# Kernel optimization log

Hardware: AMD Instinct MI355X
Metric: run time of the kernel (lower is better)

Reference implementation:

```python
import jax, jax.numpy as jnp
import numpy as np
from jax.scipy.special import logsumexp


def _lstm(x, mask, Wk, Wr, b, reverse=False):
    # x: [B,T,D], mask: [B,T] bool. Keras LSTM defaults: gate order i,f,g,o,
    # sigmoid recurrent activation, tanh activation. Masked steps carry state.
    if reverse:
        x = x[:, ::-1]
        mask = mask[:, ::-1]
    B, T, _ = x.shape
    H = Wr.shape[0]
    xz = jnp.einsum('btd,dh->bth', x, Wk) + b  # [B,T,4H] input projections, done once

    def step(carry, inp):
        h, c = carry
        z_t, m = inp  # [B,4H], [B]
        z = z_t + h @ Wr
        i, f, g, o = jnp.split(z, 4, axis=-1)
        i = jax.nn.sigmoid(i)
        f = jax.nn.sigmoid(f)
        g = jnp.tanh(g)
        o = jax.nn.sigmoid(o)
        c_new = f * c + i * g
        h_new = o * jnp.tanh(c_new)
        m = m[:, None]
        h = jnp.where(m, h_new, h)
        c = jnp.where(m, c_new, c)
        return (h, c), h

    h0 = jnp.zeros((B, H), x.dtype)
    (_, _), hs = jax.lax.scan(step, (h0, h0), (xz.transpose(1, 0, 2), mask.T))
    hs = hs.transpose(1, 0, 2)  # [B,T,H]
    if reverse:
        hs = hs[:, ::-1]
    return hs


def _crf_log_likelihood(logits, tags, lengths, trans):
    # TFA crf_log_likelihood: sequence_score - log_norm (forward algorithm)
    B, T, C = logits.shape
    t_idx = jnp.arange(T)
    mask = t_idx[None, :] < lengths[:, None]  # [B,T]
    # unary score: sum_t logits[b,t,tags[b,t]] over valid t
    unary = jnp.take_along_axis(logits, tags[..., None], axis=2)[..., 0]
    unary = jnp.sum(jnp.where(mask, unary, 0.0), axis=1)
    # binary score: sum_t trans[tags[t], tags[t+1]] for t < len-1
    binary = trans[tags[:, :-1], tags[:, 1:]]  # [B,T-1]
    mask2 = t_idx[None, : T - 1] < (lengths - 1)[:, None]
    binary = jnp.sum(jnp.where(mask2, binary, 0.0), axis=1)
    # log normalizer via forward algorithm scan
    alpha0 = logits[:, 0]  # [B,C]

    def step(alpha, inp):
        logit_t, m = inp  # [B,C], [B]
        new = logsumexp(alpha[:, :, None] + trans[None], axis=1) + logit_t
        alpha = jnp.where(m[:, None], new, alpha)
        return alpha, None

    alpha, _ = jax.lax.scan(step, alpha0,
                            (logits[:, 1:].transpose(1, 0, 2), mask[:, 1:].T))
    log_norm = logsumexp(alpha, axis=1)
    return unary + binary - log_norm


def setup_inputs() -> dict:
    key = jax.random.key(0)
    ks = jax.random.split(key, 12)
    V, D, H, C, B, T = 30000, 300, 256, 9, 64, 512
    lengths = jax.random.randint(ks[0], (B,), T // 4, T + 1).astype(jnp.int32)
    valid = jnp.arange(T)[None, :] < lengths[:, None]
    inputs = (jax.random.randint(ks[1], (B, T), 1, V) * valid).astype(jnp.int32)
    targets = (jax.random.randint(ks[2], (B, T), 0, C) * valid).astype(jnp.int32)
    s = 0.05
    return {
        'inputs': inputs,
        'inputs_length': lengths,
        'targets': targets,
        'embedding': jax.random.normal(ks[3], (V, D), jnp.float32) * s,
        'Wk_f': jax.random.normal(ks[4], (D, 4 * H), jnp.float32) * s,
        'Wr_f': jax.random.normal(ks[5], (H, 4 * H), jnp.float32) * s,
        'b_f': jnp.zeros((4 * H,), jnp.float32),
        'Wk_b': jax.random.normal(ks[6], (D, 4 * H), jnp.float32) * s,
        'Wr_b': jax.random.normal(ks[7], (H, 4 * H), jnp.float32) * s,
        'b_b': jnp.zeros((4 * H,), jnp.float32),
        'dense_W': jax.random.normal(ks[8], (2 * H, C), jnp.float32) * s,
        'dense_b': jnp.zeros((C,), jnp.float32),
        'trans': jax.random.uniform(ks[9], (C, C), jnp.float32),
    }


def reference(inputs, inputs_length, targets, embedding, Wk_f, Wr_f, b_f,
              Wk_b, Wr_b, b_b, dense_W, dense_b, trans):
    T = inputs.shape[1]
    mask = jnp.arange(T)[None, :] < inputs_length[:, None]  # [B,T]
    emb = embedding[inputs]  # [B,T,D] (dropout is identity in inference)
    h_f = _lstm(emb, mask, Wk_f, Wr_f, b_f, reverse=False)
    h_b = _lstm(emb, mask, Wk_b, Wr_b, b_b, reverse=True)
    h = jnp.concatenate([h_f, h_b], axis=-1)  # [B,T,2H]
    logits = h @ dense_W + dense_b  # [B,T,C]
    log_likelihood = _crf_log_likelihood(logits, targets, inputs_length, trans)
    return logits, log_likelihood, trans
```

## Files before the change

### kernel.cpp

```cpp
#include <hip/hip_runtime.h>
#include <cstdint>
#include <cstddef>

typedef unsigned int  u32;
typedef unsigned short u16;
typedef _Float16 f16;
typedef _Float16 f16x2 __attribute__((ext_vector_type(2)));
typedef _Float16 half8 __attribute__((ext_vector_type(8)));
typedef float    f32x4v __attribute__((ext_vector_type(4)));
typedef int      i32x4 __attribute__((ext_vector_type(4)));

#define BATCH 64
#define TSEQ  512
#define DEMB  300
#define KPAD  320
#define HDIM  256
#define G4    1024
#define NCLS  9

__device__ __forceinline__ u32 packf16(float a, float b) {
  f16x2 v; v.x = (f16)a; v.y = (f16)b;
  return __builtin_bit_cast(u32, v);
}
__device__ __forceinline__ float f16f(u16 x) {
  return (float)__builtin_bit_cast(f16, x);
}
__device__ __forceinline__ float sigm_fast(float x) {
  return __builtin_amdgcn_rcpf(1.f + __expf(-x));
}
__device__ __forceinline__ float tanh_fast(float x) {
  float ax = __builtin_fabsf(x);
  float e = __expf(-2.f * ax);
  float t = (1.f - e) * __builtin_amdgcn_rcpf(1.f + e);
  return copysignf(t, x);
}
__device__ __forceinline__ int sdot4(int a, int b, int c) {
#if __has_builtin(__builtin_amdgcn_sdot4)
  return __builtin_amdgcn_sdot4(a, b, c, false);
#else
  int r;
  asm volatile("v_dot4_i32_i8 %0, %1, %2, %3" : "=v"(r) : "v"(a), "v"(b), "v"(c));
  return r;
#endif
}

__global__ __launch_bounds__(256) void embcvt_k(const float* __restrict__ emb,
                                                u16* __restrict__ out) {
  const int v  = blockIdx.x * 16 + (threadIdx.x >> 4);
  const int kc = threadIdx.x & 15;
  u32* __restrict__ dst = (u32*)(out + (size_t)v * KPAD + kc * 20);
  if (kc < 15) {
    const float* __restrict__ src = emb + (size_t)v * DEMB + kc * 20;
    float tmp[20];
#pragma unroll
    for (int j = 0; j < 20; ++j) tmp[j] = src[j];
#pragma unroll
    for (int j = 0; j < 10; ++j) dst[j] = packf16(tmp[2 * j], tmp[2 * j + 1]);
  } else {
#pragma unroll
    for (int j = 0; j < 10; ++j) dst[j] = 0u;
  }
}

__global__ __launch_bounds__(256) void wkt_k(const float* __restrict__ Wk_f,
                                             const float* __restrict__ Wk_b,
                                             u16* __restrict__ wkt) {
  const int dir = blockIdx.y;
  const float* __restrict__ Wk = dir ? Wk_b : Wk_f;
  const int col = blockIdx.x * 16 + (threadIdx.x >> 4);
  const int kc  = threadIdx.x & 15;
  u32* __restrict__ dst = (u32*)(wkt + ((size_t)dir * G4 + col) * KPAD + kc * 20);
  if (kc < 15) {
    float tmp[20];
#pragma unroll
    for (int j = 0; j < 20; ++j) tmp[j] = Wk[(size_t)(kc * 20 + j) * G4 + col];
#pragma unroll
    for (int j = 0; j < 10; ++j) dst[j] = packf16(tmp[2 * j], tmp[2 * j + 1]);
  } else {
#pragma unroll
    for (int j = 0; j < 10; ++j) dst[j] = 0u;
  }
}

__global__ __launch_bounds__(256) void wr8_k(const float* __restrict__ Wr_f,
                                             const float* __restrict__ Wr_b,
                                             signed char* __restrict__ wr8) {
  const int dir = blockIdx.y;
  const float* __restrict__ Wr = dir ? Wr_b : Wr_f;
  const int col = blockIdx.x * 16 + (threadIdx.x >> 4);
  const int k0  = (threadIdx.x & 15) * 16;
  float tmp[16];
#pragma unroll
  for (int j = 0; j < 16; ++j) tmp[j] = Wr[(size_t)(k0 + j) * G4 + col];
  u32 pw[4];
#pragma unroll
  for (int jj = 0; jj < 4; ++jj) {
    u32 p = 0;
#pragma unroll
    for (int b = 0; b < 4; ++b) {
      int q = (int)__builtin_rintf(tmp[4 * jj + b] * 512.f);
      q = q > 127 ? 127 : (q < -127 ? -127 : q);
      p |= ((u32)(q & 255)) << (8 * b);
    }
    pw[jj] = p;
  }
  *(uint4*)(wr8 + ((size_t)dir * G4 + col) * HDIM + k0) =
      make_uint4(pw[0], pw[1], pw[2], pw[3]);
}

__global__ __launch_bounds__(256) void xz_gemm_k(
    const int* __restrict__ inputs, const u16* __restrict__ wkt,
    const u16* __restrict__ embf16, const float* __restrict__ b_f,
    const float* __restrict__ b_b, u16* __restrict__ xz)
{
  __shared__ __align__(16) u16 As[128 * 40];
  __shared__ __align__(16) u16 Bs[128 * 40];
  const int tid  = threadIdx.x;
  const int wv   = tid >> 6, lane = tid & 63;
  const int quad = lane >> 4, fl = lane & 15;
  const int cbi  = blockIdx.x;
  const int dir  = cbi >> 3;
  const int cb1  = (cbi & 7) * 128;
  const int rb   = blockIdx.y * 128;
  const float* __restrict__ bias = dir ? b_b : b_f;

  const int sm = tid >> 1, sh = (tid & 1) * 16;
  const int vrow = inputs[rb + sm];
  const u16* __restrict__ asrc = wkt + ((size_t)(dir * G4) + cb1 + sm) * KPAD + sh;
  const u16* __restrict__ bsrc = embf16 + (size_t)vrow * KPAD + sh;

  f32x4v acc[2][8];
#pragma unroll
  for (int bt = 0; bt < 2; ++bt)
#pragma unroll
    for (int i = 0; i < 8; ++i) acc[bt][i] = (f32x4v){0.f, 0.f, 0.f, 0.f};

  for (int kt = 0; kt < 10; ++kt) {
    const int k0 = kt * 32;
    uint4 a0v = *(const uint4*)(asrc + k0);
    uint4 a1v = *(const uint4*)(asrc + k0 + 8);
    uint4 b0v = *(const uint4*)(bsrc + k0);
    uint4 b1v = *(const uint4*)(bsrc + k0 + 8);
    *(uint4*)&As[sm * 40 + sh]     = a0v;
    *(uint4*)&As[sm * 40 + sh + 8] = a1v;
    *(uint4*)&Bs[sm * 40 + sh]     = b0v;
    *(uint4*)&Bs[sm * 40 + sh + 8] = b1v;
    __syncthreads();
    half8 bf[2];
#pragma unroll
    for (int bt = 0; bt < 2; ++bt)
      bf[bt] = *(const half8*)&Bs[(wv * 32 + bt * 16 + fl) * 40 + quad * 8];
#pragma unroll
    for (int i = 0; i < 8; ++i) {
      half8 af = *(const half8*)&As[(i * 16 + fl) * 40 + quad * 8];
      acc[0][i] = __builtin_amdgcn_mfma_f32_16x16x32_f16(af, bf[0], acc[0][i], 0, 0, 0);
      acc[1][i] = __builtin_amdgcn_mfma_f32_16x16x32_f16(af, bf[1], acc[1][i], 0, 0, 0);
    }
    __syncthreads();
  }
#pragma unroll
  for (int bt = 0; bt < 2; ++bt) {
    const int row = rb + wv * 32 + bt * 16 + fl;
    u16* __restrict__ orow = xz + ((size_t)(dir * BATCH * TSEQ) + row) * G4;
#pragma unroll
    for (int i = 0; i < 8; ++i) {
      const int mb = cb1 + i * 16 + quad * 4;
      const float4 bb = *(const float4*)&bias[mb];
      f32x4v v = acc[bt][i];
      uint2 pk;
      pk.x = packf16(v[0] + bb.x, v[1] + bb.y);
      pk.y = packf16(v[2] + bb.z, v[3] + bb.w);
      *(uint2*)&orow[mb] = pk;
    }
  }
}

#define PIN2(a, b) asm volatile("" : "+v"(a), "+v"(b))
__global__ __launch_bounds__(512, 2) void lstm_k(
    const u16* __restrict__ xz, const signed char* __restrict__ wr8,
    const int* __restrict__ lengths, u16* __restrict__ hcat)
{
  const int chain = blockIdx.x;
  const int dir   = chain >> 6;
  const int batch = chain & 63;
  const int tid   = threadIdx.x;
  const int odd   = tid & 1;
  const int hidx  = tid >> 1;
  const int c0    = odd * 256 + hidx;
  const int c1    = c0 + 512;
  const float DEQ = 1.f / (512.f * 127.f);

  __shared__ __align__(16) signed char hpk[2][256];

  const signed char* __restrict__ wr8w = wr8 + (size_t)dir * G4 * HDIM;

  i32x4 w0[16], w1[16];
#pragma unroll
  for (int j = 0; j < 16; ++j) {
    w0[j] = *(const i32x4*)(wr8w + (size_t)c0 * HDIM + j * 16);
    w1[j] = *(const i32x4*)(wr8w + (size_t)c1 * HDIM + j * 16);
  }

  if (tid < 256) hpk[0][tid] = 0;

  float c = 0.f, h = 0.f;
  const int len = lengths[batch];
  const u16* __restrict__ xzb = xz + (size_t)(dir * BATCH + batch) * TSEQ * G4;
  u16* __restrict__ hrow = hcat + (size_t)batch * TSEQ * 512 + dir * 256;
  __syncthreads();

  int tt = dir ? (TSEQ - 1) : 0;
  const int dt = dir ? -1 : 1;
  const long xstride = (long)dt * G4;
  const long hstride = (long)dt * 512;
  const u16* xp = xzb + (size_t)tt * G4;
  u16* hp = hrow + (size_t)tt * 512;
  u16 x0 = xp[c0];
  u16 x1 = xp[c1];

  for (int st = 0; st < TSEQ; ++st) {
#pragma unroll
    for (int j = 0; j < 16; j += 2) {
      PIN2(w0[j], w0[j + 1]);
      PIN2(w1[j], w1[j + 1]);
    }
    const u16* xpn = (st == TSEQ - 1) ? xp : (xp + xstride);
    u16 xn0 = xpn[c0];
    u16 xn1 = xpn[c1];

    const int par = st & 1;
    const signed char* hb = &hpk[par][0];

    int a0p = 0, a0q = 0, a1p = 0, a1q = 0;
#pragma unroll
    for (int ch = 0; ch < 4; ++ch) {
      i32x4 hv[4];
#pragma unroll
      for (int q = 0; q < 4; ++q)
        hv[q] = *(const i32x4*)(hb + ch * 64 + q * 16);
#pragma unroll
      for (int q = 0; q < 4; ++q) {
#pragma unroll
        for (int e = 0; e < 4; ++e) {
          if (((q * 4 + e) & 1) == 0) {
            a0p = sdot4(hv[q][e], w0[ch * 4 + q][e], a0p);
            a1p = sdot4(hv[q][e], w1[ch * 4 + q][e], a1p);
          } else {
            a0q = sdot4(hv[q][e], w0[ch * 4 + q][e], a0q);
            a1q = sdot4(hv[q][e], w1[ch * 4 + q][e], a1q);
          }
        }
      }
    }
    const int s0 = a0p + a0q;
    const int s1 = a1p + a1q;

    float z0 = (float)s0 * DEQ + f16f(x0);
    float z1 = (float)s1 * DEQ + f16f(x1);
    float g0 = sigm_fast(z0);
    float earg = odd ? -z1 : (-2.f * __builtin_fabsf(z1));
    float e = __expf(earg);
    float d = __builtin_amdgcn_rcpf(1.f + e);
    float g1 = odd ? d : copysignf((1.f - e) * d, z1);

    float P = g0 * g1;
    float Pin = __shfl_xor(P, 1);
    if (odd) {
      float cn = fmaf(g0, c, Pin);
      float hn = g1 * tanh_fast(cn);
      if (tt < len) { c = cn; h = hn; }
      u32 hb2 = packf16(h, h);
      hp[hidx] = (u16)(hb2 & 0xffffu);
      int hq = (int)__builtin_rintf(h * 127.f);
      hpk[par ^ 1][hidx] = (signed char)hq;
    }
    __syncthreads();
    x0 = xn0; x1 = xn1; tt += dt;
    xp = xpn;
    if (st != TSEQ - 1) hp += hstride;
  }
}

__global__ __launch_bounds__(256) void dense_k(
    const u16* __restrict__ hcat, const float* __restrict__ W,
    const float* __restrict__ bias, float* __restrict__ out)
{
  const int lane = threadIdx.x & 63;
  const int wv = threadIdx.x >> 6;
  const int rowbase = (blockIdx.x * 4 + wv) * 8;
  for (int rr = 0; rr < 8; ++rr) {
    const int row = rowbase + rr;
    const u16* __restrict__ hr = hcat + (size_t)row * 512;
    float hv[8];
#pragma unroll
    for (int i = 0; i < 8; ++i)
      hv[i] = f16f(hr[i * 64 + lane]);
    float myout = 0.f;
#pragma unroll
    for (int cc = 0; cc < 9; ++cc) {
      float p = 0.f;
#pragma unroll
      for (int i = 0; i < 8; ++i)
        p = fmaf(hv[i], W[(size_t)(i * 64 + lane) * 9 + cc], p);
#pragma unroll
      for (int o = 32; o > 0; o >>= 1) p += __shfl_xor(p, o);
      if (lane == cc) myout = p + bias[cc];
    }
    if (lane < 9) out[(size_t)row * 9 + lane] = myout;
  }
}

__global__ __launch_bounds__(64) void crf_k(
    const float* __restrict__ logits, const int* __restrict__ tags,
    const int* __restrict__ lengths, const float* __restrict__ trans,
    float* __restrict__ out_ll, float* __restrict__ out_trans)
{
  const int b = blockIdx.x;
  const int lane = threadIdx.x;
  const int len = lengths[b];
  const float* __restrict__ lg = logits + (size_t)b * TSEQ * NCLS;
  const int* __restrict__ tg = tags + (size_t)b * TSEQ;

  float ua = 0.f, ba = 0.f;
  for (int t = lane; t < TSEQ; t += 64) {
    int tag = tg[t];
    if (t < len) ua += lg[t * 9 + tag];
    if (t < len - 1) ba += trans[tag * 9 + tg[t + 1]];
  }
  float s = ua + ba;
#pragma unroll
  for (int o = 32; o > 0; o >>= 1) s += __shfl_xor(s, o);

  const int j = (lane < 9) ? lane : 0;
  float trc[9], alpha[9];
#pragma unroll
  for (int i = 0; i < 9; ++i) trc[i] = trans[i * 9 + j];
#pragma unroll
  for (int i = 0; i < 9; ++i) alpha[i] = lg[i];
  for (int t = 1; t < TSEQ; ++t) {
    if (t >= len) break;
    float m = -1e30f;
#pragma unroll
    for (int i = 0; i < 9; ++i) m = fmaxf(m, alpha[i] + trc[i]);
    float ss = 0.f;
#pragma unroll
    for (int i = 0; i < 9; ++i) ss += __expf(alpha[i] + trc[i] - m);
    float nj = __logf(ss) + m + lg[t * 9 + j];
#pragma unroll
    for (int i = 0; i < 9; ++i) alpha[i] = __shfl(nj, i);
  }
  float m2 = -1e30f;
#pragma unroll
  for (int i = 0; i < 9; ++i) m2 = fmaxf(m2, alpha[i]);
  float s2 = 0.f;
#pragma unroll
  for (int i = 0; i < 9; ++i) s2 += __expf(alpha[i] - m2);
  float lse = __logf(s2) + m2;
  if (lane == 0) out_ll[b] = s - lse;
  if (b == 0)
    for (int i = lane; i < 81; i += 64) out_trans[i] = trans[i];
}

extern "C" void kernel_launch(void* const* d_in, const int* in_sizes, int n_in,
                              void* d_out, int out_size, void* d_ws, size_t ws_size,
                              hipStream_t stream)
{
  const int*   inputs  = (const int*)d_in[0];
  const int*   lengths = (const int*)d_in[1];
  const int*   targets = (const int*)d_in[2];
  const float* emb     = (const float*)d_in[3];
  const float* Wk_f    = (const float*)d_in[4];
  const float* Wr_f    = (const float*)d_in[5];
  const float* b_f     = (const float*)d_in[6];
  const float* Wk_b    = (const float*)d_in[7];
  const float* Wr_b    = (const float*)d_in[8];
  const float* b_b     = (const float*)d_in[9];
  const float* dense_W = (const float*)d_in[10];
  const float* dense_b = (const float*)d_in[11];
  const float* trans   = (const float*)d_in[12];

  char* ws = (char*)d_ws;
  u16*         wkt    = (u16*)ws;
  signed char* wr8    = (signed char*)(ws + 1310720ull);
  u16*         embf16 = (u16*)(ws + 1835008ull);
  u16*         xz     = (u16*)(ws + 1835008ull + 19200000ull);
  u16*         hcat   = (u16*)(ws + 1835008ull + 19200000ull + 134217728ull);

  float* out_logits = (float*)d_out;
  float* out_ll     = out_logits + (size_t)BATCH * TSEQ * NCLS;
  float* out_trans  = out_ll + BATCH;

  hipLaunchKernelGGL(embcvt_k, dim3(1875), dim3(256), 0, stream, emb, embf16);
  hipLaunchKernelGGL(wkt_k, dim3(64, 2), dim3(256), 0, stream, Wk_f, Wk_b, wkt);
  hipLaunchKernelGGL(wr8_k, dim3(64, 2), dim3(256), 0, stream, Wr_f, Wr_b, wr8);
  hipLaunchKernelGGL(xz_gemm_k, dim3(16, 256), dim3(256), 0, stream,
                     inputs, wkt, embf16, b_f, b_b, xz);
  hipLaunchKernelGGL(lstm_k, dim3(128), dim3(512), 0, stream,
                     xz, wr8, lengths, hcat);
  hipLaunchKernelGGL(dense_k, dim3(1024), dim3(256), 0, stream,
                     hcat, dense_W, dense_b, out_logits);
  hipLaunchKernelGGL(crf_k, dim3(64), dim3(64), 0, stream,
                     out_logits, targets, lengths, trans, out_ll, out_trans);
}
```

Measured before the change: 799.9 us.

## Split LSTM recurrence to one gate column per thread with 1024-thread blocks

The recurrent LSTM kernel now uses 1024 threads per chain instead of 512. Each thread holds one int8 weight row of 64 registers rather than two, and computes a single gate. The four gates of each hidden unit are exchanged with three xor shuffles, and the g==1 lane updates the cell state. This halves the dot-product work and register pressure per thread, shortening the serial per-step latency. In exchange it adds more shuffles and a larger block-wide barrier every step, and drops the register-pinning asm.

Result: slower. 862.8 us (+7.9%).

```diff
diff --git a/kernel.cpp b/kernel.cpp
--- a/kernel.cpp
+++ b/kernel.cpp
@@ -175,8 +175,7 @@
   }
 }
 
-#define PIN2(a, b) asm volatile("" : "+v"(a), "+v"(b))
-__global__ __launch_bounds__(512, 2) void lstm_k(
+__global__ __launch_bounds__(1024, 4) void lstm_k(
     const u16* __restrict__ xz, const signed char* __restrict__ wr8,
     const int* __restrict__ lengths, u16* __restrict__ hcat)
 {
@@ -184,22 +183,19 @@
   const int dir   = chain >> 6;
   const int batch = chain & 63;
   const int tid   = threadIdx.x;
-  const int odd   = tid & 1;
-  const int hidx  = tid >> 1;
-  const int c0    = odd * 256 + hidx;
-  const int c1    = c0 + 512;
+  const int g     = tid & 3;
+  const int hidx  = tid >> 2;
+  const int col   = g * 256 + hidx;
   const float DEQ = 1.f / (512.f * 127.f);
 
   __shared__ __align__(16) signed char hpk[2][256];
 
   const signed char* __restrict__ wr8w = wr8 + (size_t)dir * G4 * HDIM;
 
-  i32x4 w0[16], w1[16];
-#pragma unroll
-  for (int j = 0; j < 16; ++j) {
-    w0[j] = *(const i32x4*)(wr8w + (size_t)c0 * HDIM + j * 16);
-    w1[j] = *(const i32x4*)(wr8w + (size_t)c1 * HDIM + j * 16);
-  }
+  i32x4 w[16];
+#pragma unroll
+  for (int j = 0; j < 16; ++j)
+    w[j] = *(const i32x4*)(wr8w + (size_t)col * HDIM + j * 16);
 
   if (tid < 256) hpk[0][tid] = 0;
 
@@ -215,59 +211,38 @@
   const long hstride = (long)dt * 512;
   const u16* xp = xzb + (size_t)tt * G4;
   u16* hp = hrow + (size_t)tt * 512;
-  u16 x0 = xp[c0];
-  u16 x1 = xp[c1];
+  u16 x0 = xp[col];
 
   for (int st = 0; st < TSEQ; ++st) {
-#pragma unroll
-    for (int j = 0; j < 16; j += 2) {
-      PIN2(w0[j], w0[j + 1]);
-      PIN2(w1[j], w1[j + 1]);
-    }
     const u16* xpn = (st == TSEQ - 1) ? xp : (xp + xstride);
-    u16 xn0 = xpn[c0];
-    u16 xn1 = xpn[c1];
+    u16 xn0 = xpn[col];
 
     const int par = st & 1;
     const signed char* hb = &hpk[par][0];
 
-    int a0p = 0, a0q = 0, a1p = 0, a1q = 0;
-#pragma unroll
-    for (int ch = 0; ch < 4; ++ch) {
-      i32x4 hv[4];
-#pragma unroll
-      for (int q = 0; q < 4; ++q)
-        hv[q] = *(const i32x4*)(hb + ch * 64 + q * 16);
-#pragma unroll
-      for (int q = 0; q < 4; ++q) {
-#pragma unroll
-        for (int e = 0; e < 4; ++e) {
-          if (((q * 4 + e) & 1) == 0) {
-            a0p = sdot4(hv[q][e], w0[ch * 4 + q][e], a0p);
-            a1p = sdot4(hv[q][e], w1[ch * 4 + q][e], a1p);
-          } else {
-            a0q = sdot4(hv[q][e], w0[ch * 4 + q][e], a0q);
-            a1q = sdot4(hv[q][e], w1[ch * 4 + q][e], a1q);
-          }
-        }
-      }
-    }
-    const int s0 = a0p + a0q;
-    const int s1 = a1p + a1q;
-
-    float z0 = (float)s0 * DEQ + f16f(x0);
-    float z1 = (float)s1 * DEQ + f16f(x1);
-    float g0 = sigm_fast(z0);
-    float earg = odd ? -z1 : (-2.f * __builtin_fabsf(z1));
+    int a0 = 0, a1 = 0, a2 = 0, a3 = 0;
+#pragma unroll
+    for (int j = 0; j < 16; ++j) {
+      i32x4 hv = *(const i32x4*)(hb + j * 16);
+      a0 = sdot4(hv[0], w[j][0], a0);
+      a1 = sdot4(hv[1], w[j][1], a1);
+      a2 = sdot4(hv[2], w[j][2], a2);
+      a3 = sdot4(hv[3], w[j][3], a3);
+    }
+    const int s = (a0 + a1) + (a2 + a3);
+
+    float z = (float)s * DEQ + f16f(x0);
+    float earg = (g == 2) ? (-2.f * __builtin_fabsf(z)) : -z;
     float e = __expf(earg);
     float d = __builtin_amdgcn_rcpf(1.f + e);
-    float g1 = odd ? d : copysignf((1.f - e) * d, z1);
-
-    float P = g0 * g1;
-    float Pin = __shfl_xor(P, 1);
-    if (odd) {
-      float cn = fmaf(g0, c, Pin);
-      float hn = g1 * tanh_fast(cn);
+    float act = (g == 2) ? copysignf((1.f - e) * d, z) : d;
+
+    float ri = __shfl_xor(act, 1);
+    float rg = __shfl_xor(act, 3);
+    float ro = __shfl_xor(act, 2);
+    if (g == 1) {
+      float cn = fmaf(act, c, ri * rg);
+      float hn = ro * tanh_fast(cn);
       if (tt < len) { c = cn; h = hn; }
       u32 hb2 = packf16(h, h);
       hp[hidx] = (u16)(hb2 & 0xffffu);
@@ -275,7 +250,7 @@
       hpk[par ^ 1][hidx] = (signed char)hq;
     }
     __syncthreads();
-    x0 = xn0; x1 = xn1; tt += dt;
+    x0 = xn0; tt += dt;
     xp = xpn;
     if (st != TSEQ - 1) hp += hstride;
   }
@@ -395,7 +370,7 @@
   hipLaunchKernelGGL(wr8_k, dim3(64, 2), dim3(256), 0, stream, Wr_f, Wr_b, wr8);
   hipLaunchKernelGGL(xz_gemm_k, dim3(16, 256), dim3(256), 0, stream,
                      inputs, wkt, embf16, b_f, b_b, xz);
-  hipLaunchKernelGGL(lstm_k, dim3(128), dim3(512), 0, stream,
+  hipLaunchKernelGGL(lstm_k, dim3(128), dim3(1024), 0, stream,
                      xz, wr8, lengths, hcat);
   hipLaunchKernelGGL(dense_k, dim3(1024), dim3(256), 0, stream,
                      hcat, dense_W, dense_b, out_logits);
```
